# Kernel optimization log

Measured on AMD Instinct MI355X. Metric: run time of the kernel, lower is better.

## Reference

```python
import jax, jax.numpy as jnp
import numpy as np

N_NODES = 100000
N_EDGES = 3200000
D_FEAT = 256
UNITS = 256


def setup_inputs() -> dict:
    key = jax.random.key(0)
    k1, k2, k3, k4, k5 = jax.random.split(key, 5)
    edge_row = jax.random.randint(k1, (N_EDGES,), 0, N_NODES, dtype=jnp.int32)
    edge_col = jax.random.randint(k2, (N_EDGES,), 0, N_NODES, dtype=jnp.int32)
    edge_val = jax.random.uniform(k3, (N_EDGES,), dtype=jnp.float32)
    x = jax.random.normal(k4, (N_NODES, D_FEAT), dtype=jnp.float32)
    weight = jax.random.normal(k5, (D_FEAT, UNITS), dtype=jnp.float32) * (1.0 / np.sqrt(D_FEAT))
    bias = jnp.zeros((UNITS,), dtype=jnp.float32)
    return {"edge_row": edge_row, "edge_col": edge_col, "edge_val": edge_val,
            "x": x, "weight": weight, "bias": bias}


def reference(edge_row, edge_col, edge_val, x, weight, bias):
    # h = X @ W  -- dense feature transform (N, units)
    h = x @ weight
    # out = An @ h -- SpMM over COO adjacency: out[r] += val_e * h[c_e]
    msgs = edge_val[:, None] * h[edge_col]          # (E, units) gather + scale
    out = jax.ops.segment_sum(msgs, edge_row, num_segments=N_NODES)
    out = out + bias
    return jax.nn.relu(out)
```

## Files before the change

kernel.cpp:

```cpp
#include <hip/hip_runtime.h>
#include <hip/hip_bf16.h>

#define N_NODES 100000
#define N_EDGES 3200000
#define DFEAT 256
#define UNITS 256

#define CHUNK 512
#define CHUNK_SHIFT 9
#define NCHUNKS ((N_NODES + CHUNK - 1) / CHUNK)

#define BIN_TILE 2048
#define BIN_NWG ((N_EDGES + BIN_TILE - 1) / BIN_TILE)
#define PADC 208

typedef short bf16x8 __attribute__((ext_vector_type(8)));
typedef float f32x4 __attribute__((ext_vector_type(4)));

__device__ __forceinline__ unsigned short f2bf(float f) {
    union { float f; unsigned u; } v; v.f = f;
    unsigned u = v.u;
    u += 0x7FFFu + ((u >> 16) & 1u);
    return (unsigned short)(u >> 16);
}

__global__ __launch_bounds__(256) void convert_x(const float4* __restrict__ x4,
                                                 unsigned short* __restrict__ xh) {
    size_t i = (size_t)blockIdx.x * 256 + threadIdx.x;
    float4 v = x4[i];
    ushort4 o = make_ushort4(f2bf(v.x), f2bf(v.y), f2bf(v.z), f2bf(v.w));
    *(ushort4*)&xh[i * 4] = o;
}

__global__ void convert_w(const float* __restrict__ w, unsigned short* __restrict__ wt) {
    int n = blockIdx.x, k = threadIdx.x;
    wt[n * DFEAT + k] = f2bf(w[k * UNITS + n]);
}

__global__ __launch_bounds__(256) void chunk_hist(const int* __restrict__ erow,
                                                  int* __restrict__ hist_all) {
    __shared__ int h[256];
    const int tid = threadIdx.x;
    h[tid] = 0;
    __syncthreads();
    const int base = blockIdx.x * BIN_TILE;
#pragma unroll
    for (int j = 0; j < 8; ++j) {
        int e = base + j * 256 + tid;
        if (e < N_EDGES) atomicAdd(&h[erow[e] >> CHUNK_SHIFT], 1);
    }
    __syncthreads();
    if (tid < NCHUNKS) hist_all[blockIdx.x * PADC + tid] = h[tid];
}

__global__ __launch_bounds__(256) void col_scan(int* __restrict__ hist_all,
                                                int* __restrict__ chunk_cnt) {
    __shared__ int t[256];
    const int b = blockIdx.x;
    const int tid = threadIdx.x;
    int v[7]; int local = 0;
#pragma unroll
    for (int j = 0; j < 7; ++j) {
        int w = tid * 7 + j;
        v[j] = (w < BIN_NWG) ? hist_all[w * PADC + b] : 0;
        local += v[j];
    }
    t[tid] = local;
    __syncthreads();
    for (int off = 1; off < 256; off <<= 1) {
        int u = 0;
        if (tid >= off) u = t[tid - off];
        __syncthreads();
        if (tid >= off) t[tid] += u;
        __syncthreads();
    }
    int run = t[tid] - local;
#pragma unroll
    for (int j = 0; j < 7; ++j) {
        int w = tid * 7 + j;
        if (w < BIN_NWG) { hist_all[w * PADC + b] = run; run += v[j]; }
    }
    if (tid == 255) chunk_cnt[b] = t[255];
}

__global__ void scan_chunks(const int* __restrict__ chunk_cnt, int* __restrict__ csum) {
    __shared__ int t[256];
    const int tid = threadIdx.x;
    int v = (tid < NCHUNKS) ? chunk_cnt[tid] : 0;
    t[tid] = v;
    __syncthreads();
    for (int off = 1; off < 256; off <<= 1) {
        int u = 0;
        if (tid >= off) u = t[tid - off];
        __syncthreads();
        if (tid >= off) t[tid] += u;
        __syncthreads();
    }
    if (tid < NCHUNKS) csum[tid] = t[tid] - v;
}

__global__ __launch_bounds__(256) void bin_edges(const int* __restrict__ erow,
                                                 const int* __restrict__ ecol,
                                                 const float* __restrict__ eval,
                                                 const int* __restrict__ hist_all,
                                                 const int* __restrict__ csum,
                                                 uint2* __restrict__ bin) {
    __shared__ int hist[256];
    __shared__ int scnt[256];
    __shared__ int delta[256];
    __shared__ uint2 rec[BIN_TILE];
    const int tid = threadIdx.x;
    const int base = blockIdx.x * BIN_TILE;

    hist[tid] = 0;
    __syncthreads();

    int r[8]; unsigned pk[8];
#pragma unroll
    for (int j = 0; j < 8; ++j) {
        int e = base + j * 256 + tid;
        if (e < N_EDGES) {
            r[j] = erow[e];
            pk[j] = (((unsigned)ecol[e]) << 15) | (f2bf(eval[e]) & 0x7FFFu);
            atomicAdd(&hist[r[j] >> CHUNK_SHIFT], 1);
        } else {
            r[j] = -1;
        }
    }
    __syncthreads();

    const int cntb = hist[tid];
    for (int off = 1; off < 256; off <<= 1) {
        int u = 0;
        if (tid >= off) u = hist[tid - off];
        __syncthreads();
        if (tid >= off) hist[tid] += u;
        __syncthreads();
    }
    const int excl = hist[tid] - cntb;
    if (tid < NCHUNKS)
        delta[tid] = csum[tid] + hist_all[blockIdx.x * PADC + tid] - excl;
    scnt[tid] = 0;
    __syncthreads();

#pragma unroll
    for (int j = 0; j < 8; ++j) {
        if (r[j] >= 0) {
            int b = r[j] >> CHUNK_SHIFT;
            int s = (b ? hist[b - 1] : 0) + atomicAdd(&scnt[b], 1);
            rec[s] = make_uint2(pk[j], (unsigned)r[j]);
        }
    }
    __syncthreads();

    const int n = min(BIN_TILE, N_EDGES - base);
    for (int s = tid; s < n; s += 256) {
        uint2 q = rec[s];
        bin[delta[(int)q.y >> CHUNK_SHIFT] + s] = q;
    }
}

__global__ __launch_bounds__(512) void sort_chunk(const int* __restrict__ csum,
                                                  const uint2* __restrict__ bin,
                                                  int* __restrict__ row_ptr,
                                                  unsigned* __restrict__ cv) {
    __shared__ int h[CHUNK];
    const int b = blockIdx.x;
    const int tid = threadIdx.x;
    const int start = csum[b];
    const int end = (b + 1 < NCHUNKS) ? csum[b + 1] : N_EDGES;

    h[tid] = 0;
    __syncthreads();
    {
        int i = start + tid;
        for (; i + 3 * 512 < end; i += 4 * 512) {
            int r0 = (int)bin[i].y, r1 = (int)bin[i + 512].y;
            int r2 = (int)bin[i + 1024].y, r3 = (int)bin[i + 1536].y;
            atomicAdd(&h[r0 & (CHUNK - 1)], 1);
            atomicAdd(&h[r1 & (CHUNK - 1)], 1);
            atomicAdd(&h[r2 & (CHUNK - 1)], 1);
            atomicAdd(&h[r3 & (CHUNK - 1)], 1);
        }
        for (; i < end; i += 512)
            atomicAdd(&h[(int)bin[i].y & (CHUNK - 1)], 1);
    }
    __syncthreads();

    const int cnt = h[tid];
    for (int off = 1; off < 512; off <<= 1) {
        int u = 0;
        if (tid >= off) u = h[tid - off];
        __syncthreads();
        if (tid >= off) h[tid] += u;
        __syncthreads();
    }
    const int rp = start + h[tid] - cnt;
    const int row = (b << CHUNK_SHIFT) + tid;
    if (row < N_NODES) row_ptr[row] = rp;
    if (b == NCHUNKS - 1 && tid == 0) row_ptr[N_NODES] = N_EDGES;
    h[tid] = rp;
    __syncthreads();

    int i = start + tid;
    for (; i + 3 * 512 < end; i += 4 * 512) {
        uint2 q0 = bin[i], q1 = bin[i + 512], q2 = bin[i + 1024], q3 = bin[i + 1536];
        int p0 = atomicAdd(&h[(int)q0.y & (CHUNK - 1)], 1);
        int p1 = atomicAdd(&h[(int)q1.y & (CHUNK - 1)], 1);
        int p2 = atomicAdd(&h[(int)q2.y & (CHUNK - 1)], 1);
        int p3 = atomicAdd(&h[(int)q3.y & (CHUNK - 1)], 1);
        cv[p0] = q0.x; cv[p1] = q1.x; cv[p2] = q2.x; cv[p3] = q3.x;
    }
    for (; i < end; i += 512) {
        uint2 q = bin[i];
        int p = atomicAdd(&h[(int)q.y & (CHUNK - 1)], 1);
        cv[p] = q.x;
    }
}

__global__ __launch_bounds__(256) void gather_rows(const int* __restrict__ row_ptr,
                                                   const unsigned* __restrict__ cv,
                                                   const unsigned short* __restrict__ xh,
                                                   unsigned short* __restrict__ tmp) {
    const int row = blockIdx.x * 4 + (threadIdx.x >> 6);
    if (row >= N_NODES) return;
    const int lane = threadIdx.x & 63;
    const int start = row_ptr[row];
    const int deg = row_ptr[row + 1] - start;
    const unsigned* __restrict__ p = cv + start;
    const uint2* __restrict__ x2 = (const uint2*)xh;

    float a0 = 0.f, a1 = 0.f, a2 = 0.f, a3 = 0.f;
    int i = 0;
    for (; i + 7 < deg; i += 8) {
        unsigned e[8]; uint2 g[8];
#pragma unroll
        for (int j = 0; j < 8; ++j) e[j] = p[i + j];
#pragma unroll
        for (int j = 0; j < 8; ++j) g[j] = x2[(size_t)(e[j] >> 15) * 64 + lane];
#pragma unroll
        for (int j = 0; j < 8; ++j) {
            float v = __uint_as_float((e[j] & 0x7FFFu) << 16);
            a0 = fmaf(v, __uint_as_float(g[j].x << 16), a0);
            a1 = fmaf(v, __uint_as_float(g[j].x & 0xFFFF0000u), a1);
            a2 = fmaf(v, __uint_as_float(g[j].y << 16), a2);
            a3 = fmaf(v, __uint_as_float(g[j].y & 0xFFFF0000u), a3);
        }
    }
    for (; i + 3 < deg; i += 4) {
        unsigned e[4]; uint2 g[4];
#pragma unroll
        for (int j = 0; j < 4; ++j) e[j] = p[i + j];
#pragma unroll
        for (int j = 0; j < 4; ++j) g[j] = x2[(size_t)(e[j] >> 15) * 64 + lane];
#pragma unroll
        for (int j = 0; j < 4; ++j) {
            float v = __uint_as_float((e[j] & 0x7FFFu) << 16);
            a0 = fmaf(v, __uint_as_float(g[j].x << 16), a0);
            a1 = fmaf(v, __uint_as_float(g[j].x & 0xFFFF0000u), a1);
            a2 = fmaf(v, __uint_as_float(g[j].y << 16), a2);
            a3 = fmaf(v, __uint_as_float(g[j].y & 0xFFFF0000u), a3);
        }
    }
    for (; i < deg; ++i) {
        unsigned e0 = p[i];
        uint2 g0 = x2[(size_t)(e0 >> 15) * 64 + lane];
        float v0 = __uint_as_float((e0 & 0x7FFFu) << 16);
        a0 = fmaf(v0, __uint_as_float(g0.x << 16), a0);
        a1 = fmaf(v0, __uint_as_float(g0.x & 0xFFFF0000u), a1);
        a2 = fmaf(v0, __uint_as_float(g0.y << 16), a2);
        a3 = fmaf(v0, __uint_as_float(g0.y & 0xFFFF0000u), a3);
    }
    ushort4 o = make_ushort4(f2bf(a0), f2bf(a1), f2bf(a2), f2bf(a3));
    *(ushort4*)&tmp[(size_t)row * 256 + lane * 4] = o;
}

#define GBM 64
#define GBK 64
#define LDK 72

__global__ __launch_bounds__(256) void gemm_mfma(
    const unsigned short* __restrict__ A,
    const unsigned short* __restrict__ Bt,
    const float* __restrict__ bias,
    float* __restrict__ C, int M)
{
    __shared__ unsigned short As[GBM * LDK];
    __shared__ unsigned short Bs[UNITS * LDK];

    const int tid = threadIdx.x;
    const int lane = tid & 63;
    const int wave_n = tid >> 6;
    const int block_m = blockIdx.x * GBM;

    const int quad = lane >> 4;
    const int l16 = lane & 15;

    const int ar = tid >> 2;
    const int aseg = tid & 3;

    f32x4 acc[4][4];
#pragma unroll
    for (int i = 0; i < 4; ++i)
#pragma unroll
        for (int j = 0; j < 4; ++j)
            acc[i][j] = {0.f, 0.f, 0.f, 0.f};

    for (int k0 = 0; k0 < DFEAT; k0 += GBK) {
        {
            const int gm = block_m + ar;
            uint4 v0 = {}, v1 = {};
            if (gm < M) {
                const uint4* src = (const uint4*)(A + (size_t)gm * DFEAT + k0 + aseg * 16);
                v0 = src[0]; v1 = src[1];
            }
            uint4* dst = (uint4*)&As[ar * LDK + aseg * 16];
            dst[0] = v0; dst[1] = v1;
        }
        {
            const uint4* src = (const uint4*)(Bt + (size_t)tid * DFEAT + k0);
            uint4* dst = (uint4*)&Bs[tid * LDK];
            uint4 v0 = src[0], v1 = src[1], v2 = src[2], v3 = src[3];
            uint4 v4 = src[4], v5 = src[5], v6 = src[6], v7 = src[7];
            dst[0] = v0; dst[1] = v1; dst[2] = v2; dst[3] = v3;
            dst[4] = v4; dst[5] = v5; dst[6] = v6; dst[7] = v7;
        }
        __syncthreads();

#pragma unroll
        for (int kc = 0; kc < 2; ++kc) {
            const int ko = kc * 32 + quad * 8;
            bf16x8 af[4], bfr[4];
#pragma unroll
            for (int i = 0; i < 4; ++i)
                af[i] = *(const bf16x8*)&As[(i * 16 + l16) * LDK + ko];
#pragma unroll
            for (int j = 0; j < 4; ++j)
                bfr[j] = *(const bf16x8*)&Bs[(wave_n * 64 + j * 16 + l16) * LDK + ko];
#pragma unroll
            for (int i = 0; i < 4; ++i)
#pragma unroll
                for (int j = 0; j < 4; ++j)
                    acc[i][j] = __builtin_amdgcn_mfma_f32_16x16x32_bf16(
                        af[i], bfr[j], acc[i][j], 0, 0, 0);
        }
        __syncthreads();
    }

#pragma unroll
    for (int j = 0; j < 4; ++j) {
        const int n = wave_n * 64 + j * 16 + l16;
        const float bj = bias[n];
#pragma unroll
        for (int i = 0; i < 4; ++i) {
            const int m0 = block_m + i * 16 + quad * 4;
#pragma unroll
            for (int rg = 0; rg < 4; ++rg) {
                const int m = m0 + rg;
                if (m < M)
                    C[(size_t)m * UNITS + n] = fmaxf(acc[i][j][rg] + bj, 0.f);
            }
        }
    }
}

extern "C" void kernel_launch(void* const* d_in, const int* in_sizes, int n_in,
                              void* d_out, int out_size, void* d_ws, size_t ws_size,
                              hipStream_t stream) {
    const int*   erow = (const int*)d_in[0];
    const int*   ecol = (const int*)d_in[1];
    const float* eval = (const float*)d_in[2];
    const float* x    = (const float*)d_in[3];
    const float* w    = (const float*)d_in[4];
    const float* bias = (const float*)d_in[5];
    float* out = (float*)d_out;

    char* ws = (char*)d_ws;
    unsigned short* tmp       = (unsigned short*)(ws);
    int*            row_ptr   = (int*)(ws + 51200000);
    int*            csum      = (int*)(ws + 51600016);
    int*            chunk_cnt = (int*)(ws + 51601040);
    unsigned*       cv        = (unsigned*)(ws + 51602064);
    unsigned short* wt        = (unsigned short*)(ws + 64402064);
    uint2*          bin       = (uint2*)(ws + 64533136);
    int*            hist_all  = (int*)(ws + 90133136);

    unsigned short* xh = (unsigned short*)d_out;

    convert_x<<<(N_NODES * DFEAT / 4) / 256, 256, 0, stream>>>((const float4*)x, xh);
    convert_w<<<UNITS, DFEAT, 0, stream>>>(w, wt);

    chunk_hist<<<BIN_NWG, 256, 0, stream>>>(erow, hist_all);
    col_scan<<<NCHUNKS, 256, 0, stream>>>(hist_all, chunk_cnt);
    scan_chunks<<<1, 256, 0, stream>>>(chunk_cnt, csum);
    bin_edges<<<BIN_NWG, 256, 0, stream>>>(erow, ecol, eval, hist_all, csum, bin);
    sort_chunk<<<NCHUNKS, 512, 0, stream>>>(csum, bin, row_ptr, cv);

    gather_rows<<<(N_NODES + 3) / 4, 256, 0, stream>>>(row_ptr, cv, xh, tmp);

    gemm_mfma<<<(N_NODES + GBM - 1) / GBM, 256, 0, stream>>>(tmp, wt, bias, out, N_NODES);
}
```

Measured before the change: 537.7 us.

## Load full A tile into LDS once, read B from global, fuse conversions

The GEMM now stages the whole 64x256 A tile in LDS in a single pass and reads the transposed weight fragments straight from global/L2 instead of staging them through LDS each K step. This removes the per-K-step barriers and the LDS copy of B, at the cost of uncoalesced-ish global reads of B per wave. The x and w conversion kernels are merged into one launch to save a launch. An extra barrier is added in sort_chunk to fix a read/write race on the shared histogram.

```diff
diff --git a/kernel.cpp b/kernel.cpp
--- a/kernel.cpp
+++ b/kernel.cpp
@@ -24,17 +24,19 @@
     return (unsigned short)(u >> 16);
 }
 
-__global__ __launch_bounds__(256) void convert_x(const float4* __restrict__ x4,
-                                                 unsigned short* __restrict__ xh) {
-    size_t i = (size_t)blockIdx.x * 256 + threadIdx.x;
-    float4 v = x4[i];
-    ushort4 o = make_ushort4(f2bf(v.x), f2bf(v.y), f2bf(v.z), f2bf(v.w));
-    *(ushort4*)&xh[i * 4] = o;
-}
-
-__global__ void convert_w(const float* __restrict__ w, unsigned short* __restrict__ wt) {
-    int n = blockIdx.x, k = threadIdx.x;
-    wt[n * DFEAT + k] = f2bf(w[k * UNITS + n]);
+__global__ __launch_bounds__(256) void convert_xw(const float4* __restrict__ x4,
+                                                  unsigned short* __restrict__ xh,
+                                                  const float* __restrict__ w,
+                                                  unsigned short* __restrict__ wt) {
+    if (blockIdx.x < 25000) {
+        size_t i = (size_t)blockIdx.x * 256 + threadIdx.x;
+        float4 v = x4[i];
+        ushort4 o = make_ushort4(f2bf(v.x), f2bf(v.y), f2bf(v.z), f2bf(v.w));
+        *(ushort4*)&xh[i * 4] = o;
+    } else {
+        int n = blockIdx.x - 25000, k = threadIdx.x;
+        wt[n * DFEAT + k] = f2bf(w[k * UNITS + n]);
+    }
 }
 
 __global__ __launch_bounds__(256) void chunk_hist(const int* __restrict__ erow,
@@ -199,6 +201,7 @@
     const int row = (b << CHUNK_SHIFT) + tid;
     if (row < N_NODES) row_ptr[row] = rp;
     if (b == NCHUNKS - 1 && tid == 0) row_ptr[N_NODES] = N_EDGES;
+    __syncthreads();
     h[tid] = rp;
     __syncthreads();
 
@@ -276,8 +279,7 @@
 }
 
 #define GBM 64
-#define GBK 64
-#define LDK 72
+#define LDK2 264
 
 __global__ __launch_bounds__(256) void gemm_mfma(
     const unsigned short* __restrict__ A,
@@ -285,8 +287,7 @@
     const float* __restrict__ bias,
     float* __restrict__ C, int M)
 {
-    __shared__ unsigned short As[GBM * LDK];
-    __shared__ unsigned short Bs[UNITS * LDK];
+    __shared__ unsigned short As[GBM * LDK2];
 
     const int tid = threadIdx.x;
     const int lane = tid & 63;
@@ -296,8 +297,21 @@
     const int quad = lane >> 4;
     const int l16 = lane & 15;
 
-    const int ar = tid >> 2;
-    const int aseg = tid & 3;
+    {
+        const int ar = tid >> 2;
+        const int seg = tid & 3;
+        const int gm = block_m + ar;
+        uint4 v[8] = {};
+        if (gm < M) {
+            const uint4* src = (const uint4*)(A + (size_t)gm * DFEAT + seg * 64);
+#pragma unroll
+            for (int j = 0; j < 8; ++j) v[j] = src[j];
+        }
+        uint4* dst = (uint4*)&As[ar * LDK2 + seg * 64];
+#pragma unroll
+        for (int j = 0; j < 8; ++j) dst[j] = v[j];
+    }
+    __syncthreads();
 
     f32x4 acc[4][4];
 #pragma unroll
@@ -306,45 +320,22 @@
         for (int j = 0; j < 4; ++j)
             acc[i][j] = {0.f, 0.f, 0.f, 0.f};
 
-    for (int k0 = 0; k0 < DFEAT; k0 += GBK) {
-        {
-            const int gm = block_m + ar;
-            uint4 v0 = {}, v1 = {};
-            if (gm < M) {
-                const uint4* src = (const uint4*)(A + (size_t)gm * DFEAT + k0 + aseg * 16);
-                v0 = src[0]; v1 = src[1];
-            }
-            uint4* dst = (uint4*)&As[ar * LDK + aseg * 16];
-            dst[0] = v0; dst[1] = v1;
-        }
-        {
-            const uint4* src = (const uint4*)(Bt + (size_t)tid * DFEAT + k0);
-            uint4* dst = (uint4*)&Bs[tid * LDK];
-            uint4 v0 = src[0], v1 = src[1], v2 = src[2], v3 = src[3];
-            uint4 v4 = src[4], v5 = src[5], v6 = src[6], v7 = src[7];
-            dst[0] = v0; dst[1] = v1; dst[2] = v2; dst[3] = v3;
-            dst[4] = v4; dst[5] = v5; dst[6] = v6; dst[7] = v7;
-        }
-        __syncthreads();
-
-#pragma unroll
-        for (int kc = 0; kc < 2; ++kc) {
-            const int ko = kc * 32 + quad * 8;
-            bf16x8 af[4], bfr[4];
-#pragma unroll
-            for (int i = 0; i < 4; ++i)
-                af[i] = *(const bf16x8*)&As[(i * 16 + l16) * LDK + ko];
+#pragma unroll
+    for (int ks = 0; ks < 8; ++ks) {
+        const int ko = ks * 32 + quad * 8;
+        bf16x8 af[4], bfr[4];
+#pragma unroll
+        for (int i = 0; i < 4; ++i)
+            af[i] = *(const bf16x8*)&As[(i * 16 + l16) * LDK2 + ko];
+#pragma unroll
+        for (int j = 0; j < 4; ++j)
+            bfr[j] = *(const bf16x8*)&Bt[(size_t)(wave_n * 64 + j * 16 + l16) * DFEAT + ko];
+#pragma unroll
+        for (int i = 0; i < 4; ++i)
 #pragma unroll
             for (int j = 0; j < 4; ++j)
-                bfr[j] = *(const bf16x8*)&Bs[(wave_n * 64 + j * 16 + l16) * LDK + ko];
-#pragma unroll
-            for (int i = 0; i < 4; ++i)
-#pragma unroll
-                for (int j = 0; j < 4; ++j)
-                    acc[i][j] = __builtin_amdgcn_mfma_f32_16x16x32_bf16(
-                        af[i], bfr[j], acc[i][j], 0, 0, 0);
-        }
-        __syncthreads();
+                acc[i][j] = __builtin_amdgcn_mfma_f32_16x16x32_bf16(
+                    af[i], bfr[j], acc[i][j], 0, 0, 0);
     }
 
 #pragma unroll
@@ -387,8 +378,7 @@
 
     unsigned short* xh = (unsigned short*)d_out;
 
-    convert_x<<<(N_NODES * DFEAT / 4) / 256, 256, 0, stream>>>((const float4*)x, xh);
-    convert_w<<<UNITS, DFEAT, 0, stream>>>(w, wt);
+    convert_xw<<<25000 + UNITS, 256, 0, stream>>>((const float4*)x, xh, w, wt);
 
     chunk_hist<<<BIN_NWG, 256, 0, stream>>>(erow, hist_all);
     col_scan<<<NCHUNKS, 256, 0, stream>>>(hist_all, chunk_cnt);
```

Result: slower. 555.4 us (+3.3%).
